# Optimization experiments

Measured on AMD Instinct MI355X. Metric: run time of the kernel, lower is better.

Reference implementation:

```python
import jax, jax.numpy as jnp
import numpy as np

EMBED_DIM = 1024
NUM_HEADS = 16
DIM_HEAD = EMBED_DIM // NUM_HEADS


def setup_inputs() -> dict:
    key = jax.random.key(0)
    ks = jax.random.split(key, 9)
    s = 1.0 / np.sqrt(EMBED_DIM)
    x = jax.random.normal(ks[0], (2, 2048, EMBED_DIM), dtype=jnp.float32)
    Wq = jax.random.uniform(ks[1], (EMBED_DIM, EMBED_DIM), jnp.float32, -s, s)
    bq = jax.random.uniform(ks[2], (EMBED_DIM,), jnp.float32, -s, s)
    Wk = jax.random.uniform(ks[3], (EMBED_DIM, EMBED_DIM), jnp.float32, -s, s)
    bk = jax.random.uniform(ks[4], (EMBED_DIM,), jnp.float32, -s, s)
    Wv = jax.random.uniform(ks[5], (EMBED_DIM, EMBED_DIM), jnp.float32, -s, s)
    bv = jax.random.uniform(ks[6], (EMBED_DIM,), jnp.float32, -s, s)
    Wo = jax.random.uniform(ks[7], (EMBED_DIM, EMBED_DIM), jnp.float32, -s, s)
    bo = jax.random.uniform(ks[8], (EMBED_DIM,), jnp.float32, -s, s)
    return {"x": x, "Wq": Wq, "bq": bq, "Wk": Wk, "bk": bk,
            "Wv": Wv, "bv": bv, "Wo": Wo, "bo": bo}


def reference(x, Wq, bq, Wk, bk, Wv, bv, Wo, bo):
    B, S, _ = x.shape
    # Linear layers (torch nn.Linear: x @ W.T + b), reshape to heads
    Q = (x @ Wq.T + bq).reshape(B, S, NUM_HEADS, DIM_HEAD)
    K = (x @ Wk.T + bk).reshape(B, S, NUM_HEADS, DIM_HEAD)
    V = (x @ Wv.T + bv).reshape(B, S, NUM_HEADS, DIM_HEAD)
    scores = jnp.einsum('bqhd,bkhd->bhqk', Q, K) / np.sqrt(DIM_HEAD)
    attn = jax.nn.softmax(scores, axis=-1)
    context = jnp.einsum('bhqk,bkhd->bqhd', attn, V).reshape(B, S, EMBED_DIM)
    return context @ Wo.T + bo
```

## Files before the change

kernel.cpp:

```cpp
#include <hip/hip_runtime.h>
#include <hip/hip_bf16.h>

#define SEQ   2048
#define EMB   1024
#define NHEAD 16
#define DHEAD 64
#define BATCH 2
#define MTOT  (BATCH*SEQ)
#define QT    64
#define KT    64
#define NTILE (SEQ/KT)

typedef __attribute__((ext_vector_type(8))) short s8v;
typedef __attribute__((ext_vector_type(4))) short s4v;
typedef __attribute__((ext_vector_type(4))) float f4v;

__device__ __forceinline__ short f2b(float f) {
    union { float fl; unsigned u; } v; v.fl = f;
    unsigned u = v.u;
    u = (u + 0x7fffu + ((u >> 16) & 1u)) >> 16;
    return (short)u;
}
__device__ __forceinline__ unsigned pk2(float a, float b) {
    union { __hip_bfloat162 h; unsigned u; } c;
    c.h = __float22bfloat162_rn(float2{a, b});
    return c.u;
}

#if __has_builtin(__builtin_amdgcn_exp2f)
__device__ __forceinline__ float exp2_fast(float x) { return __builtin_amdgcn_exp2f(x); }
#else
__device__ __forceinline__ float exp2_fast(float x) { return exp2f(x); }
#endif

__device__ __forceinline__ void pl32swap(unsigned &a, unsigned &b) {
    asm("v_permlane32_swap_b32 %0, %1" : "+v"(a), "+v"(b));
}
__device__ __forceinline__ void pl16swap(unsigned &a, unsigned &b) {
    asm("v_permlane16_swap_b32 %0, %1" : "+v"(a), "+v"(b));
}

__device__ __forceinline__ void bar_lds() {
    asm volatile("s_waitcnt lgkmcnt(0)\n\ts_barrier" ::: "memory");
}

__device__ __forceinline__ void gl_lds16(const short* g, short* l) {
    __builtin_amdgcn_global_load_lds(
        (const __attribute__((address_space(1))) void*)g,
        (__attribute__((address_space(3))) void*)l, 16, 0, 0);
}

__global__ __launch_bounds__(256)
void cvt_swz(const float* __restrict__ s0, const float* __restrict__ s1,
             const float* __restrict__ s2, const float* __restrict__ s3,
             const float* __restrict__ s4,
             short* __restrict__ d0, short* __restrict__ d1,
             short* __restrict__ d2, short* __restrict__ d3,
             short* __restrict__ d4)
{
    const int seg = blockIdx.y;
    const float* s = seg == 0 ? s0 : seg == 1 ? s1 : seg == 2 ? s2 : seg == 3 ? s3 : s4;
    short*       d = seg == 0 ? d0 : seg == 1 ? d1 : seg == 2 ? d2 : seg == 3 ? d3 : d4;
    const int nchunk = (seg == 0 ? MTOT * EMB : EMB * EMB) / 8;
    const int stride = gridDim.x * 256;
    for (int i = blockIdx.x * 256 + threadIdx.x; i < nchunk; i += stride) {
        const int row = i >> 7;
        const int c   = i & 127;
        const float4 v0 = *(const float4*)(s + (size_t)i * 8);
        const float4 v1 = *(const float4*)(s + (size_t)i * 8 + 4);
        s8v o;
        o[0] = f2b(v0.x); o[1] = f2b(v0.y); o[2] = f2b(v0.z); o[3] = f2b(v0.w);
        o[4] = f2b(v1.x); o[5] = f2b(v1.y); o[6] = f2b(v1.z); o[7] = f2b(v1.w);
        const int cp = (c & ~7) | ((c & 7) ^ (row & 7));
        *(s8v*)(d + (size_t)row * EMB + cp * 8) = o;
    }
}

template<int NT, bool FUSED3>
__global__ __launch_bounds__(256, 3)
void gemm_bb3(const short* __restrict__ A,
              const short* __restrict__ W0, const short* __restrict__ W1, const short* __restrict__ W2,
              const float* __restrict__ B0, const float* __restrict__ B1, const float* __restrict__ B2,
              void* __restrict__ C0, void* __restrict__ C1, void* __restrict__ C2)
{
    constexpr int JN = NT / 32;
    const int K = EMB, N = EMB;
    const int ntiles = EMB / NT;
    const int mat = blockIdx.x / ntiles;
    const int n0  = (blockIdx.x % ntiles) * NT;
    const int m0  = blockIdx.y * 128;
    const short* W  = (mat == 0) ? W0 : (mat == 1 ? W1 : W2);
    const float* Bi = (mat == 0) ? B0 : (mat == 1 ? B1 : B2);
    void*        C  = (mat == 0) ? C0 : (mat == 1 ? C1 : C2);
    const float qscale = (FUSED3 && mat == 0) ? 0.18033688f : 1.0f;

    __shared__ __align__(16) short As[128 * 64];
    __shared__ __align__(16) short Ws[NT * 64];

    const int tid  = threadIdx.x;
    const int lane = tid & 63;
    const int wave = tid >> 6;
    const int quad = lane >> 4;
    const int l16  = lane & 15;
    const int l8   = l16 & 7;
    const int wm   = wave >> 1;
    const int wn   = wave & 1;

    f4v acc[4][JN] = {};

    const int srow = lane >> 3;
    const int scol = (lane & 7) * 8;

    for (int k0 = 0; k0 < K; k0 += 64) {
        #pragma unroll
        for (int p = 0; p < 4; ++p) {
            const int rbase = wave * 32 + p * 8;
            gl_lds16(A + (size_t)(m0 + rbase + srow) * K + k0 + scol,
                     As + rbase * 64);
        }
        #pragma unroll
        for (int p = 0; p < NT / 32; ++p) {
            const int rbase = wave * (NT / 4) + p * 8;
            gl_lds16(W + (size_t)(n0 + rbase + srow) * K + k0 + scol,
                     Ws + rbase * 64);
        }
        __syncthreads();

        #pragma unroll
        for (int kk = 0; kk < 2; ++kk) {
            const int slot = ((kk * 4 + quad) ^ l8) * 8;
            s8v af[4], wf[JN];
            #pragma unroll
            for (int i = 0; i < 4; ++i)
                af[i] = *(const s8v*)(As + (wm * 64 + i * 16 + l16) * 64 + slot);
            #pragma unroll
            for (int j = 0; j < JN; ++j)
                wf[j] = *(const s8v*)(Ws + (wn * (NT / 2) + j * 16 + l16) * 64 + slot);
            #pragma unroll
            for (int i = 0; i < 4; ++i)
                #pragma unroll
                for (int j = 0; j < JN; ++j)
                    acc[i][j] = __builtin_amdgcn_mfma_f32_16x16x32_bf16(
                        af[i], wf[j], acc[i][j], 0, 0, 0);
        }
        __syncthreads();
    }

    #pragma unroll
    for (int j = 0; j < JN; ++j) {
        const int n = n0 + wn * (NT / 2) + j * 16 + l16;
        const float bv = Bi[n];
        #pragma unroll
        for (int i = 0; i < 4; ++i) {
            const int mb = m0 + wm * 64 + i * 16 + quad * 4;
            if (FUSED3 && mat == 2) {
                const int bb = mb >> 11, s = mb & 2047;
                s4v ov;
                #pragma unroll
                for (int rr = 0; rr < 4; ++rr) ov[rr] = f2b(acc[i][j][rr] + bv);
                *(s4v*)((short*)C + ((size_t)(bb * 1024 + n)) * SEQ + s) = ov;
            } else if (FUSED3) {
                #pragma unroll
                for (int rr = 0; rr < 4; ++rr)
                    ((short*)C)[(size_t)(mb + rr) * N + n] = f2b((acc[i][j][rr] + bv) * qscale);
            } else {
                #pragma unroll
                for (int rr = 0; rr < 4; ++rr)
                    ((float*)C)[(size_t)(mb + rr) * N + n] = acc[i][j][rr] + bv;
            }
        }
    }
}

__global__ __launch_bounds__(256, 4)
void attn_mfma9(const short* Q, const short* __restrict__ Kg,
                const short* __restrict__ Vt, short* O)
{
    const int i    = blockIdx.x;
    const int xcd  = i & 7;
    const int slot = i >> 3;
    const int combo = xcd * 4 + (slot >> 5);
    const int qb = slot & 31;
    const int h  = combo & 15;
    const int b  = combo >> 4;
    const int q0 = qb * QT;

    const int tid  = threadIdx.x;
    const int lane = tid & 63;
    const int wave = tid >> 6;
    const int quad = lane >> 4;
    const int l16  = lane & 15;
    const int l8   = l16 & 7;

    __shared__ __align__(16) short Ks[2][64 * 64];
    __shared__ __align__(16) short Vs[2][64 * 64];

    s8v qf[2];
    #pragma unroll
    for (int kk = 0; kk < 2; ++kk)
        qf[kk] = *(const s8v*)(Q + (size_t)(b * SEQ + q0 + wave * 16 + l16) * EMB
                                 + h * DHEAD + kk * 32 + quad * 8);

    f4v oacc[4] = {};
    f4v sacc    = {};
    s8v onef;
    #pragma unroll
    for (int e = 0; e < 8; ++e) onef[e] = (short)0x3F80;

    const int r = lane >> 3, c = lane & 7;
    const int sc8 = (c ^ r) * 8;
    const bool isK = wave < 2;
    const int wrow = (wave & 1) * 32;
    const size_t kbase = (size_t)(b * SEQ) * EMB + h * DHEAD;
    const size_t vbase = (size_t)((b * NHEAD + h) * DHEAD) * SEQ;
    const short* gsrc = isK ? Kg + kbase + (size_t)(wrow + r) * EMB + sc8
                            : Vt + vbase + (size_t)(wrow + r) * SEQ + sc8;
    const size_t grow8 = isK ? (size_t)8 * EMB : (size_t)8 * SEQ;
    const size_t tstep = isK ? (size_t)KT * EMB : (size_t)KT;
    short* const lbase = (isK ? (short*)Ks : (short*)Vs) + wrow * 64;

    #pragma unroll
    for (int p = 0; p < 4; ++p)
        gl_lds16(gsrc + p * grow8, lbase + p * 8 * 64);
    const short* gnext = gsrc + tstep;

    for (int t = 0; t < NTILE; ++t) {
        const int buf = t & 1;
        __syncthreads();
        if (t + 1 < NTILE) {
            short* ldst = lbase + (buf ^ 1) * (64 * 64);
            #pragma unroll
            for (int p = 0; p < 4; ++p)
                gl_lds16(gnext + p * grow8, ldst + p * 8 * 64);
            gnext += tstep;
        }
        const short* KsB = Ks[buf];
        const short* VsB = Vs[buf];

        f4v sc[4] = {};
        __builtin_amdgcn_s_setprio(1);
        #pragma unroll
        for (int kk = 0; kk < 2; ++kk) {
            const int ko = ((kk * 4 + quad) ^ l8) * 8;
            s8v kf[4];
            #pragma unroll
            for (int j = 0; j < 4; ++j)
                kf[j] = *(const s8v*)(KsB + (j * 16 + l16) * 64 + ko);
            #pragma unroll
            for (int j = 0; j < 4; ++j)
                sc[j] = __builtin_amdgcn_mfma_f32_16x16x32_bf16(
                    kf[j], qf[kk], sc[j], 0, 0, 0);
        }
        __builtin_amdgcn_s_setprio(0);

        unsigned u[4][2];
        #pragma unroll
        for (int j = 0; j < 4; ++j) {
            u[j][0] = pk2(exp2_fast(sc[j][0]), exp2_fast(sc[j][1]));
            u[j][1] = pk2(exp2_fast(sc[j][2]), exp2_fast(sc[j][3]));
        }

        #pragma unroll
        for (int r2 = 0; r2 < 2; ++r2) {
            pl32swap(u[0][r2], u[1][r2]);
            pl32swap(u[2][r2], u[3][r2]);
            pl16swap(u[0][r2], u[1][r2]);
            pl16swap(u[2][r2], u[3][r2]);
        }
        union { unsigned uu[4]; s8v s; } pfa, pfb;
        pfa.uu[0] = u[0][0]; pfa.uu[1] = u[0][1]; pfa.uu[2] = u[1][0]; pfa.uu[3] = u[1][1];
        pfb.uu[0] = u[2][0]; pfb.uu[1] = u[2][1]; pfb.uu[2] = u[3][0]; pfb.uu[3] = u[3][1];

        __builtin_amdgcn_s_setprio(1);
        #pragma unroll
        for (int kk = 0; kk < 2; ++kk) {
            const s8v pf = kk ? pfb.s : pfa.s;
            sacc = __builtin_amdgcn_mfma_f32_16x16x32_bf16(onef, pf, sacc, 0, 0, 0);
            const int ko = ((kk * 4 + quad) ^ l8) * 8;
            #pragma unroll
            for (int j = 0; j < 4; ++j) {
                const s8v vf = *(const s8v*)(VsB + (j * 16 + l16) * 64 + ko);
                oacc[j] = __builtin_amdgcn_mfma_f32_16x16x32_bf16(
                    vf, pf, oacc[j], 0, 0, 0);
            }
        }
        __builtin_amdgcn_s_setprio(0);
    }

    const float inv = 1.0f / sacc[0];

    __syncthreads();
    short* Os = (short*)Ks;
    #pragma unroll
    for (int j = 0; j < 4; ++j) {
        union { unsigned uu[2]; s4v s; } ov;
        ov.uu[0] = pk2(oacc[j][0] * inv, oacc[j][1] * inv);
        ov.uu[1] = pk2(oacc[j][2] * inv, oacc[j][3] * inv);
        const int pc = ((j * 2 + (quad >> 1)) ^ l8) * 8 + (quad & 1) * 4;
        *(s4v*)(Os + (wave * 16 + l16) * 64 + pc) = ov.s;
    }
    bar_lds();

    const int row = tid >> 2;
    const int cb  = (tid & 3) * 2;
    #pragma unroll
    for (int c4 = 0; c4 < 2; ++c4) {
        const int pcc = cb + c4;
        const s8v tt = *(const s8v*)(Os + row * 64 + pcc * 8);
        *(s8v*)(O + (size_t)(b * SEQ + q0 + row) * EMB + h * DHEAD + pcc * 8) = tt;
    }
}

extern "C" void kernel_launch(void* const* d_in, const int* in_sizes, int n_in,
                              void* d_out, int out_size, void* d_ws, size_t ws_size,
                              hipStream_t stream)
{
    const float* x  = (const float*)d_in[0];
    const float* Wq = (const float*)d_in[1];
    const float* bq = (const float*)d_in[2];
    const float* Wk = (const float*)d_in[3];
    const float* bk = (const float*)d_in[4];
    const float* Wv = (const float*)d_in[5];
    const float* bv = (const float*)d_in[6];
    const float* Wo = (const float*)d_in[7];
    const float* bo = (const float*)d_in[8];
    float* out = (float*)d_out;

    short* xb  = (short*)d_ws;
    short* Wqb = xb  + (size_t)MTOT * EMB;
    short* Wkb = Wqb + (size_t)EMB * EMB;
    short* Wvb = Wkb + (size_t)EMB * EMB;
    short* Wob = Wvb + (size_t)EMB * EMB;
    short* Qw  = Wob + (size_t)EMB * EMB;
    short* Kw  = Qw  + (size_t)MTOT * EMB;
    short* Vtw = Kw  + (size_t)MTOT * EMB;

    cvt_swz<<<dim3(512, 5), 256, 0, stream>>>(x, Wq, Wk, Wv, Wo,
                                              xb, Wqb, Wkb, Wvb, Wob);

    gemm_bb3<128, true><<<dim3(24, 32), 256, 0, stream>>>(
        xb, Wqb, Wkb, Wvb, bq, bk, bv, Qw, Kw, Vtw);

    attn_mfma9<<<dim3(BATCH * NHEAD * (SEQ / QT)), 256, 0, stream>>>(Qw, Kw, Vtw, Qw);

    gemm_bb3<64, false><<<dim3(16, 32), 256, 0, stream>>>(
        Qw, Wob, Wob, Wob, bo, bo, bo, out, out, out);
}
```

Measured before the change: 183.5 us.

## Switch attention to 32x32x16 MFMA with 128-row query tiles

```diff
diff --git a/kernel.cpp b/kernel.cpp
--- a/kernel.cpp
+++ b/kernel.cpp
@@ -7,13 +7,14 @@
 #define DHEAD 64
 #define BATCH 2
 #define MTOT  (BATCH*SEQ)
-#define QT    64
+#define QT    128
 #define KT    64
 #define NTILE (SEQ/KT)
 
 typedef __attribute__((ext_vector_type(8))) short s8v;
 typedef __attribute__((ext_vector_type(4))) short s4v;
 typedef __attribute__((ext_vector_type(4))) float f4v;
+typedef __attribute__((ext_vector_type(16))) float f16v;
 
 __device__ __forceinline__ short f2b(float f) {
     union { float fl; unsigned u; } v; v.fl = f;
@@ -35,9 +36,6 @@
 
 __device__ __forceinline__ void pl32swap(unsigned &a, unsigned &b) {
     asm("v_permlane32_swap_b32 %0, %1" : "+v"(a), "+v"(b));
-}
-__device__ __forceinline__ void pl16swap(unsigned &a, unsigned &b) {
-    asm("v_permlane16_swap_b32 %0, %1" : "+v"(a), "+v"(b));
 }
 
 __device__ __forceinline__ void bar_lds() {
@@ -172,45 +170,45 @@
     }
 }
 
-__global__ __launch_bounds__(256, 4)
-void attn_mfma9(const short* Q, const short* __restrict__ Kg,
-                const short* __restrict__ Vt, short* O)
+__global__ __launch_bounds__(256, 2)
+void attn_mfma10(const short* Q, const short* __restrict__ Kg,
+                 const short* __restrict__ Vt, short* O)
 {
     const int i    = blockIdx.x;
     const int xcd  = i & 7;
     const int slot = i >> 3;
-    const int combo = xcd * 4 + (slot >> 5);
-    const int qb = slot & 31;
+    const int combo = xcd * 4 + (slot >> 4);
+    const int qb = slot & 15;
     const int h  = combo & 15;
     const int b  = combo >> 4;
     const int q0 = qb * QT;
 
     const int tid  = threadIdx.x;
     const int lane = tid & 63;
-    const int wave = tid >> 6;
-    const int quad = lane >> 4;
-    const int l16  = lane & 15;
-    const int l8   = l16 & 7;
+    const int wq   = tid >> 6;
+    const int l32  = lane & 31;
+    const int hi   = lane >> 5;
+    const int l8   = l32 & 7;
 
     __shared__ __align__(16) short Ks[2][64 * 64];
     __shared__ __align__(16) short Vs[2][64 * 64];
 
-    s8v qf[2];
-    #pragma unroll
-    for (int kk = 0; kk < 2; ++kk)
-        qf[kk] = *(const s8v*)(Q + (size_t)(b * SEQ + q0 + wave * 16 + l16) * EMB
-                                 + h * DHEAD + kk * 32 + quad * 8);
-
-    f4v oacc[4] = {};
-    f4v sacc    = {};
+    s8v qf[4];
+    #pragma unroll
+    for (int ds = 0; ds < 4; ++ds)
+        qf[ds] = *(const s8v*)(Q + (size_t)(b * SEQ + q0 + wq * 32 + l32) * EMB
+                                 + h * DHEAD + ds * 16 + hi * 8);
+
+    f16v oa0 = {}, oa1 = {};
+    f16v sacc = {};
     s8v onef;
     #pragma unroll
     for (int e = 0; e < 8; ++e) onef[e] = (short)0x3F80;
 
     const int r = lane >> 3, c = lane & 7;
-    const int sc8 = (c ^ r) * 8;
-    const bool isK = wave < 2;
-    const int wrow = (wave & 1) * 32;
+    const int sc8 = (c ^ (r & 7)) * 8;
+    const bool isK = wq < 2;
+    const int wrow = (wq & 1) * 32;
     const size_t kbase = (size_t)(b * SEQ) * EMB + h * DHEAD;
     const size_t vbase = (size_t)((b * NHEAD + h) * DHEAD) * SEQ;
     const short* gsrc = isK ? Kg + kbase + (size_t)(wrow + r) * EMB + sc8
@@ -237,52 +235,45 @@
         const short* KsB = Ks[buf];
         const short* VsB = Vs[buf];
 
-        f4v sc[4] = {};
+        f16v sc0 = {}, sc1 = {};
         __builtin_amdgcn_s_setprio(1);
         #pragma unroll
-        for (int kk = 0; kk < 2; ++kk) {
-            const int ko = ((kk * 4 + quad) ^ l8) * 8;
-            s8v kf[4];
-            #pragma unroll
-            for (int j = 0; j < 4; ++j)
-                kf[j] = *(const s8v*)(KsB + (j * 16 + l16) * 64 + ko);
-            #pragma unroll
-            for (int j = 0; j < 4; ++j)
-                sc[j] = __builtin_amdgcn_mfma_f32_16x16x32_bf16(
-                    kf[j], qf[kk], sc[j], 0, 0, 0);
+        for (int ds = 0; ds < 4; ++ds) {
+            const int ko = ((ds * 2 + hi) ^ l8) * 8;
+            const s8v kf0 = *(const s8v*)(KsB + (l32)      * 64 + ko);
+            const s8v kf1 = *(const s8v*)(KsB + (32 + l32) * 64 + ko);
+            sc0 = __builtin_amdgcn_mfma_f32_32x32x16_bf16(kf0, qf[ds], sc0, 0, 0, 0);
+            sc1 = __builtin_amdgcn_mfma_f32_32x32x16_bf16(kf1, qf[ds], sc1, 0, 0, 0);
         }
         __builtin_amdgcn_s_setprio(0);
 
-        unsigned u[4][2];
-        #pragma unroll
-        for (int j = 0; j < 4; ++j) {
-            u[j][0] = pk2(exp2_fast(sc[j][0]), exp2_fast(sc[j][1]));
-            u[j][1] = pk2(exp2_fast(sc[j][2]), exp2_fast(sc[j][3]));
-        }
-
-        #pragma unroll
-        for (int r2 = 0; r2 < 2; ++r2) {
-            pl32swap(u[0][r2], u[1][r2]);
-            pl32swap(u[2][r2], u[3][r2]);
-            pl16swap(u[0][r2], u[1][r2]);
-            pl16swap(u[2][r2], u[3][r2]);
-        }
-        union { unsigned uu[4]; s8v s; } pfa, pfb;
-        pfa.uu[0] = u[0][0]; pfa.uu[1] = u[0][1]; pfa.uu[2] = u[1][0]; pfa.uu[3] = u[1][1];
-        pfb.uu[0] = u[2][0]; pfb.uu[1] = u[2][1]; pfb.uu[2] = u[3][0]; pfb.uu[3] = u[3][1];
+        unsigned u0[8], u1[8];
+        #pragma unroll
+        for (int ri = 0; ri < 8; ++ri) {
+            u0[ri] = pk2(exp2_fast(sc0[2 * ri]), exp2_fast(sc0[2 * ri + 1]));
+            u1[ri] = pk2(exp2_fast(sc1[2 * ri]), exp2_fast(sc1[2 * ri + 1]));
+        }
+
+        pl32swap(u0[0], u0[2]); pl32swap(u0[1], u0[3]);
+        pl32swap(u0[4], u0[6]); pl32swap(u0[5], u0[7]);
+        pl32swap(u1[0], u1[2]); pl32swap(u1[1], u1[3]);
+        pl32swap(u1[4], u1[6]); pl32swap(u1[5], u1[7]);
+        union { unsigned uu[4]; s8v s; } pb0, pb1, pb2, pb3;
+        pb0.uu[0] = u0[0]; pb0.uu[1] = u0[1]; pb0.uu[2] = u0[2]; pb0.uu[3] = u0[3];
+        pb1.uu[0] = u0[4]; pb1.uu[1] = u0[5]; pb1.uu[2] = u0[6]; pb1.uu[3] = u0[7];
+        pb2.uu[0] = u1[0]; pb2.uu[1] = u1[1]; pb2.uu[2] = u1[2]; pb2.uu[3] = u1[3];
+        pb3.uu[0] = u1[4]; pb3.uu[1] = u1[5]; pb3.uu[2] = u1[6]; pb3.uu[3] = u1[7];
 
         __builtin_amdgcn_s_setprio(1);
         #pragma unroll
-        for (int kk = 0; kk < 2; ++kk) {
-            const s8v pf = kk ? pfb.s : pfa.s;
-            sacc = __builtin_amdgcn_mfma_f32_16x16x32_bf16(onef, pf, sacc, 0, 0, 0);
-            const int ko = ((kk * 4 + quad) ^ l8) * 8;
-            #pragma unroll
-            for (int j = 0; j < 4; ++j) {
-                const s8v vf = *(const s8v*)(VsB + (j * 16 + l16) * 64 + ko);
-                oacc[j] = __builtin_amdgcn_mfma_f32_16x16x32_bf16(
-                    vf, pf, oacc[j], 0, 0, 0);
-            }
+        for (int ks = 0; ks < 4; ++ks) {
+            const s8v pf = ks == 0 ? pb0.s : ks == 1 ? pb1.s : ks == 2 ? pb2.s : pb3.s;
+            sacc = __builtin_amdgcn_mfma_f32_32x32x16_bf16(onef, pf, sacc, 0, 0, 0);
+            const int ko = ((ks * 2 + hi) ^ l8) * 8;
+            const s8v vf0 = *(const s8v*)(VsB + (l32)      * 64 + ko);
+            const s8v vf1 = *(const s8v*)(VsB + (32 + l32) * 64 + ko);
+            oa0 = __builtin_amdgcn_mfma_f32_32x32x16_bf16(vf0, pf, oa0, 0, 0, 0);
+            oa1 = __builtin_amdgcn_mfma_f32_32x32x16_bf16(vf1, pf, oa1, 0, 0, 0);
         }
         __builtin_amdgcn_s_setprio(0);
     }
@@ -291,20 +282,27 @@
 
     __syncthreads();
     short* Os = (short*)Ks;
-    #pragma unroll
-    for (int j = 0; j < 4; ++j) {
-        union { unsigned uu[2]; s4v s; } ov;
-        ov.uu[0] = pk2(oacc[j][0] * inv, oacc[j][1] * inv);
-        ov.uu[1] = pk2(oacc[j][2] * inv, oacc[j][3] * inv);
-        const int pc = ((j * 2 + (quad >> 1)) ^ l8) * 8 + (quad & 1) * 4;
-        *(s4v*)(Os + (wave * 16 + l16) * 64 + pc) = ov.s;
+    const int orow = wq * 32 + l32;
+    #pragma unroll
+    for (int db = 0; db < 2; ++db) {
+        #pragma unroll
+        for (int m = 0; m < 4; ++m) {
+            const float a0 = (db ? oa1[4 * m + 0] : oa0[4 * m + 0]) * inv;
+            const float a1 = (db ? oa1[4 * m + 1] : oa0[4 * m + 1]) * inv;
+            const float a2 = (db ? oa1[4 * m + 2] : oa0[4 * m + 2]) * inv;
+            const float a3 = (db ? oa1[4 * m + 3] : oa0[4 * m + 3]) * inv;
+            union { unsigned uu[2]; s4v s; } ov;
+            ov.uu[0] = pk2(a0, a1);
+            ov.uu[1] = pk2(a2, a3);
+            *(s4v*)(Os + orow * 64 + ((db * 4 + m) ^ l8) * 8 + 4 * hi) = ov.s;
+        }
     }
     bar_lds();
 
-    const int row = tid >> 2;
-    const int cb  = (tid & 3) * 2;
-    #pragma unroll
-    for (int c4 = 0; c4 < 2; ++c4) {
+    const int row = tid >> 1;
+    const int cb  = (tid & 1) * 4;
+    #pragma unroll
+    for (int c4 = 0; c4 < 4; ++c4) {
         const int pcc = cb + c4;
         const s8v tt = *(const s8v*)(Os + row * 64 + pcc * 8);
         *(s8v*)(O + (size_t)(b * SEQ + q0 + row) * EMB + h * DHEAD + pcc * 8) = tt;
@@ -341,7 +339,7 @@
     gemm_bb3<128, true><<<dim3(24, 32), 256, 0, stream>>>(
         xb, Wqb, Wkb, Wvb, bq, bk, bv, Qw, Kw, Vtw);
 
-    attn_mfma9<<<dim3(BATCH * NHEAD * (SEQ / QT)), 256, 0, stream>>>(Qw, Kw, Vtw, Qw);
+    attn_mfma10<<<dim3(BATCH * NHEAD * (SEQ / QT)), 256, 0, stream>>>(Qw, Kw, Vtw, Qw);
 
     gemm_bb3<64, false><<<dim3(16, 32), 256, 0, stream>>>(
         Qw, Wob, Wob, Wob, bo, bo, bo, out, out, out);
```

Measured after the change: 190.7 us. 1.04x slower.
